# Performance work log

Hardware: AMD Instinct MI355X
Metric: run time of the kernel (lower is better)

The kernel has to match this reference:

```python
import jax, jax.numpy as jnp
import numpy as np

R = 8
EPS = 1e-08


def diff_x(t, r):
    # t: (B,C,H,W), running cumsum along H -> windowed sum along H
    left = t[:, :, r:2 * r + 1]
    middle = t[:, :, 2 * r + 1:] - t[:, :, :-2 * r - 1]
    right = t[:, :, -1:] - t[:, :, -2 * r - 1:-r - 1]
    return jnp.concatenate([left, middle, right], axis=2)


def diff_y(t, r):
    left = t[:, :, :, r:2 * r + 1]
    middle = t[:, :, :, 2 * r + 1:] - t[:, :, :, :-2 * r - 1]
    right = t[:, :, :, -1:] - t[:, :, :, -2 * r - 1:-r - 1]
    return jnp.concatenate([left, middle, right], axis=3)


def box_filter(x, r):
    return diff_y(diff_x(jnp.cumsum(x, axis=2), r).cumsum(axis=3), r)


def bilinear_align_corners(x, H, W):
    # x: (B,C,h,w) -> (B,C,H,W), matching F.interpolate(mode='bilinear', align_corners=True)
    h, w = x.shape[2], x.shape[3]
    ys = jnp.linspace(0.0, h - 1.0, H, dtype=x.dtype)
    xs = jnp.linspace(0.0, w - 1.0, W, dtype=x.dtype)
    y0 = jnp.clip(jnp.floor(ys).astype(jnp.int32), 0, h - 1)
    x0 = jnp.clip(jnp.floor(xs).astype(jnp.int32), 0, w - 1)
    y1 = jnp.clip(y0 + 1, 0, h - 1)
    x1 = jnp.clip(x0 + 1, 0, w - 1)
    wy = (ys - y0.astype(x.dtype))[:, None]   # (H,1)
    wx = (xs - x0.astype(x.dtype))[None, :]   # (1,W)
    v00 = x[:, :, y0[:, None], x0[None, :]]
    v01 = x[:, :, y0[:, None], x1[None, :]]
    v10 = x[:, :, y1[:, None], x0[None, :]]
    v11 = x[:, :, y1[:, None], x1[None, :]]
    top = v00 * (1 - wx) + v01 * wx
    bot = v10 * (1 - wx) + v11 * wx
    return top * (1 - wy) + bot * wy


def setup_inputs() -> dict:
    key = jax.random.key(0)
    k1, k2, k3 = jax.random.split(key, 3)
    lr_x = jax.random.uniform(k1, (4, 3, 512, 512), dtype=jnp.float32)
    lr_y = jax.random.uniform(k2, (4, 3, 512, 512), dtype=jnp.float32)
    hr_x = jax.random.uniform(k3, (4, 3, 2048, 2048), dtype=jnp.float32)
    return {"lr_x": lr_x, "lr_y": lr_y, "hr_x": hr_x}


def reference(lr_x, lr_y, hr_x):
    _, _, h_lr, w_lr = lr_x.shape
    _, _, h_hr, w_hr = hr_x.shape
    N = box_filter(jnp.ones((1, 1, h_lr, w_lr), dtype=lr_x.dtype), R)
    mean_x = box_filter(lr_x, R) / N
    mean_y = box_filter(lr_y, R) / N
    cov_xy = box_filter(lr_x * lr_y, R) / N - mean_x * mean_y
    var_x = box_filter(lr_x * lr_x, R) / N - mean_x * mean_x
    A = cov_xy / (var_x + EPS)
    b = mean_y - A * mean_x
    mean_A = bilinear_align_corners(A, h_hr, w_hr)
    mean_b = bilinear_align_corners(b, h_hr, w_hr)
    return mean_A * hr_x + mean_b
```

## Files before the change

### kernel.cpp

```cpp
#include <hip/hip_runtime.h>

#define RR 8
#define TILE 32
#define EXT (TILE + 2 * RR)

typedef float f4 __attribute__((ext_vector_type(4)));

__global__ __launch_bounds__(256) void k_ab(
    const float* __restrict__ lrx, const float* __restrict__ lry,
    float* __restrict__ Aout, float* __restrict__ Bout, int H, int W) {
  __shared__ float sx[EXT][EXT];
  __shared__ float sy[EXT][EXT];
  __shared__ float hx[EXT][TILE];
  __shared__ float hy[EXT][TILE];
  __shared__ float hxy[EXT][TILE];
  __shared__ float hxx[EXT][TILE];

  const int bc = blockIdx.z;
  const size_t plane = (size_t)bc * H * W;
  const float* __restrict__ px = lrx + plane;
  const float* __restrict__ py = lry + plane;
  const int tx0 = blockIdx.x * TILE;
  const int ty0 = blockIdx.y * TILE;
  const int tid = threadIdx.y * 32 + threadIdx.x;

  const bool interior = (tx0 >= RR) && (ty0 >= RR) &&
                        (tx0 + TILE + RR <= W) && (ty0 + TILE + RR <= H);
  if (interior) {
    const size_t base = (size_t)(ty0 - RR) * W + (tx0 - RR);
    for (int i = tid; i < EXT * (EXT / 4); i += 256) {
      int r = i / (EXT / 4);
      int c4 = (i - r * (EXT / 4)) * 4;
      size_t o = base + (size_t)r * W + c4;
      *(float4*)&sx[r][c4] = *(const float4*)(px + o);
      *(float4*)&sy[r][c4] = *(const float4*)(py + o);
    }
  } else {
    for (int i = tid; i < EXT * EXT; i += 256) {
      int r = i / EXT, c = i % EXT;
      int gy = ty0 + r - RR, gx = tx0 + c - RR;
      float vx = 0.f, vy = 0.f;
      if (gy >= 0 && gy < H && gx >= 0 && gx < W) {
        size_t o = (size_t)gy * W + gx;
        vx = px[o];
        vy = py[o];
      }
      sx[r][c] = vx;
      sy[r][c] = vy;
    }
  }
  __syncthreads();

  for (int q = tid; q < EXT * (TILE / 4); q += 256) {
    int r = q >> 3;
    int c0 = (q & 7) * 4;
    float xv[20], yv[20];
#pragma unroll
    for (int t = 0; t < 5; ++t) {
      float4 x4 = *(const float4*)&sx[r][c0 + 4 * t];
      float4 y4 = *(const float4*)&sy[r][c0 + 4 * t];
      xv[4 * t + 0] = x4.x; xv[4 * t + 1] = x4.y; xv[4 * t + 2] = x4.z; xv[4 * t + 3] = x4.w;
      yv[4 * t + 0] = y4.x; yv[4 * t + 1] = y4.y; yv[4 * t + 2] = y4.z; yv[4 * t + 3] = y4.w;
    }
    float pv[20], qv[20];
#pragma unroll
    for (int i = 0; i < 20; ++i) { pv[i] = xv[i] * yv[i]; qv[i] = xv[i] * xv[i]; }
    float ax = 0.f, ay = 0.f, axy = 0.f, axx = 0.f;
#pragma unroll
    for (int i = 0; i < 17; ++i) { ax += xv[i]; ay += yv[i]; axy += pv[i]; axx += qv[i]; }
    float4 ox, oy, oxy, oxx;
    ox.x = ax; oy.x = ay; oxy.x = axy; oxx.x = axx;
#pragma unroll
    for (int j = 1; j < 4; ++j) {
      ax += xv[j + 16] - xv[j - 1];
      ay += yv[j + 16] - yv[j - 1];
      axy += pv[j + 16] - pv[j - 1];
      axx += qv[j + 16] - qv[j - 1];
      (&ox.x)[j] = ax; (&oy.x)[j] = ay; (&oxy.x)[j] = axy; (&oxx.x)[j] = axx;
    }
    *(float4*)&hx[r][c0] = ox;
    *(float4*)&hy[r][c0] = oy;
    *(float4*)&hxy[r][c0] = oxy;
    *(float4*)&hxx[r][c0] = oxx;
  }
  __syncthreads();

  const int c = threadIdx.x;
  const int r0 = threadIdx.y * 4;
  float vx[20], vy[20], vxy[20], vxx[20];
#pragma unroll
  for (int i = 0; i < 20; ++i) {
    vx[i] = hx[r0 + i][c];
    vy[i] = hy[r0 + i][c];
    vxy[i] = hxy[r0 + i][c];
    vxx[i] = hxx[r0 + i][c];
  }
  float sX = 0.f, sY = 0.f, sXY = 0.f, sXX = 0.f;
#pragma unroll
  for (int i = 0; i < 17; ++i) { sX += vx[i]; sY += vy[i]; sXY += vxy[i]; sXX += vxx[i]; }

  const int gx = tx0 + c;
  const int nx = min(gx + RR, W - 1) - max(gx - RR, 0) + 1;
#pragma unroll
  for (int j = 0; j < 4; ++j) {
    if (j > 0) {
      sX += vx[j + 16] - vx[j - 1];
      sY += vy[j + 16] - vy[j - 1];
      sXY += vxy[j + 16] - vxy[j - 1];
      sXX += vxx[j + 16] - vxx[j - 1];
    }
    const int gy = ty0 + r0 + j;
    const int ny = min(gy + RR, H - 1) - max(gy - RR, 0) + 1;
    float inv = 1.f / (float)(nx * ny);
    float mx = sX * inv;
    float my = sY * inv;
    float cov = sXY * inv - mx * my;
    float var = sXX * inv - mx * mx;
    float a = cov / (var + 1e-8f);
    float bv = my - a * mx;
    size_t o = plane + (size_t)gy * W + gx;
    Aout[o] = a;
    Bout[o] = bv;
  }
}

#define KO_LDSW 264
__global__ __launch_bounds__(256) void k_out(
    const float* __restrict__ A, const float* __restrict__ Bb,
    const float* __restrict__ hr, float* __restrict__ out,
    int hl, int wl, int Hh, int Wh) {
  __shared__ float As[3][KO_LDSW];
  __shared__ float Bs[3][KO_LDSW];

  const int yb = blockIdx.y * 4;
  const int bc = blockIdx.z;
  const int xb = blockIdx.x * 1024;

  const float scy = (float)(hl - 1) / (float)(Hh - 1);
  const float scx = (float)(wl - 1) / (float)(Wh - 1);

  int v;
  {
    float fy0 = (float)yb * scy;
    int t = (int)fy0;
    if (t > hl - 1) t = hl - 1;
    v = t;
  }

  int ry0[4], ry1[4];
  float wyv[4];
#pragma unroll
  for (int r = 0; r < 4; ++r) {
    float fy = (float)(yb + r) * scy;
    int y0 = (int)fy;
    if (y0 > hl - 1) y0 = hl - 1;
    int y1 = y0 + 1;
    if (y1 > hl - 1) y1 = hl - 1;
    wyv[r] = fy - (float)y0;
    ry0[r] = y0 - v;
    ry1[r] = y1 - v;
  }

  const int x0base = (int)((float)xb * scx);
  const size_t lrBase = (size_t)bc * hl * wl;

  for (int i = threadIdx.x; i < 3 * KO_LDSW; i += 256) {
    int rr = i / KO_LDSW;
    int cc = i - rr * KO_LDSW;
    int xl = x0base + cc;
    if (xl > wl - 1) xl = wl - 1;
    int yr = v + rr;
    if (yr > hl - 1) yr = hl - 1;
    size_t o = lrBase + (size_t)yr * wl + xl;
    As[rr][cc] = A[o];
    Bs[rr][cc] = Bb[o];
  }
  __syncthreads();

  const int xg = xb + threadIdx.x * 4;
  int li[4];
  float wxv[4];
#pragma unroll
  for (int j = 0; j < 4; ++j) {
    float fx = (float)(xg + j) * scx;
    int x0 = (int)fx;
    wxv[j] = fx - (float)x0;
    li[j] = x0 - x0base;
  }

  const size_t hrBase = ((size_t)bc * Hh + yb) * Wh + xg;
  f4 h[4];
#pragma unroll
  for (int r = 0; r < 4; ++r)
    h[r] = __builtin_nontemporal_load((const f4*)(hr + hrBase + (size_t)r * Wh));

#pragma unroll
  for (int r = 0; r < 4; ++r) {
    const float* __restrict__ a0 = As[ry0[r]];
    const float* __restrict__ a1 = As[ry1[r]];
    const float* __restrict__ b0 = Bs[ry0[r]];
    const float* __restrict__ b1 = Bs[ry1[r]];
    const float wy = wyv[r];
    f4 res;
#pragma unroll
    for (int j = 0; j < 4; ++j) {
      int l = li[j];
      float w = wxv[j];
      float a00 = a0[l], a01 = a0[l + 1];
      float a10 = a1[l], a11 = a1[l + 1];
      float c00 = b0[l], c01 = b0[l + 1];
      float c10 = b1[l], c11 = b1[l + 1];
      float at = a00 + (a01 - a00) * w;
      float ab = a10 + (a11 - a10) * w;
      float bt = c00 + (c01 - c00) * w;
      float bbv = c10 + (c11 - c10) * w;
      float a = at + (ab - at) * wy;
      float b = bt + (bbv - bt) * wy;
      res[j] = a * h[r][j] + b;
    }
    __builtin_nontemporal_store(res, (f4*)(out + hrBase + (size_t)r * Wh));
  }
}

extern "C" void kernel_launch(void* const* d_in, const int* in_sizes, int n_in,
                              void* d_out, int out_size, void* d_ws, size_t ws_size,
                              hipStream_t stream) {
  const float* lrx = (const float*)d_in[0];
  const float* lry = (const float*)d_in[1];
  const float* hrx = (const float*)d_in[2];
  float* out = (float*)d_out;

  const int BC = 12;
  const int hl = 512, wl = 512;
  const int Hh = 2048, Wh = 2048;

  float* A = (float*)d_ws;
  float* B = A + (size_t)BC * hl * wl;

  dim3 g1(wl / TILE, hl / TILE, BC);
  dim3 b1(32, 8);
  k_ab<<<g1, b1, 0, stream>>>(lrx, lry, A, B, hl, wl);

  dim3 g2(Wh / 1024, Hh / 4, BC);
  dim3 b2(256);
  k_out<<<g2, b2, 0, stream>>>(A, B, hrx, out, hl, wl, Hh, Wh);
}
```

Before: 359.7 us.

## Interleave A/b coefficients, process 8 output rows per block, issue hr loads before barrier

```diff
diff --git a/kernel.cpp b/kernel.cpp
--- a/kernel.cpp
+++ b/kernel.cpp
@@ -8,7 +8,7 @@
 
 __global__ __launch_bounds__(256) void k_ab(
     const float* __restrict__ lrx, const float* __restrict__ lry,
-    float* __restrict__ Aout, float* __restrict__ Bout, int H, int W) {
+    float2* __restrict__ ABout, int H, int W) {
   __shared__ float sx[EXT][EXT];
   __shared__ float sy[EXT][EXT];
   __shared__ float hx[EXT][TILE];
@@ -119,63 +119,39 @@
     float a = cov / (var + 1e-8f);
     float bv = my - a * mx;
     size_t o = plane + (size_t)gy * W + gx;
-    Aout[o] = a;
-    Bout[o] = bv;
+    ABout[o] = make_float2(a, bv);
   }
 }
 
+#define ROWS 8
 #define KO_LDSW 264
 __global__ __launch_bounds__(256) void k_out(
-    const float* __restrict__ A, const float* __restrict__ Bb,
-    const float* __restrict__ hr, float* __restrict__ out,
-    int hl, int wl, int Hh, int Wh) {
-  __shared__ float As[3][KO_LDSW];
-  __shared__ float Bs[3][KO_LDSW];
-
-  const int yb = blockIdx.y * 4;
+    const float2* __restrict__ AB, const float* __restrict__ hr,
+    float* __restrict__ out, int hl, int wl, int Hh, int Wh) {
+  __shared__ float2 ABs[4][KO_LDSW];
+
+  const int yb = blockIdx.y * ROWS;
   const int bc = blockIdx.z;
   const int xb = blockIdx.x * 1024;
 
   const float scy = (float)(hl - 1) / (float)(Hh - 1);
   const float scx = (float)(wl - 1) / (float)(Wh - 1);
 
-  int v;
-  {
-    float fy0 = (float)yb * scy;
-    int t = (int)fy0;
-    if (t > hl - 1) t = hl - 1;
-    v = t;
-  }
-
-  int ry0[4], ry1[4];
-  float wyv[4];
-#pragma unroll
-  for (int r = 0; r < 4; ++r) {
-    float fy = (float)(yb + r) * scy;
-    int y0 = (int)fy;
-    if (y0 > hl - 1) y0 = hl - 1;
-    int y1 = y0 + 1;
-    if (y1 > hl - 1) y1 = hl - 1;
-    wyv[r] = fy - (float)y0;
-    ry0[r] = y0 - v;
-    ry1[r] = y1 - v;
-  }
+  int v = (int)((float)yb * scy);
+  if (v > hl - 1) v = hl - 1;
 
   const int x0base = (int)((float)xb * scx);
   const size_t lrBase = (size_t)bc * hl * wl;
 
-  for (int i = threadIdx.x; i < 3 * KO_LDSW; i += 256) {
+  for (int i = threadIdx.x; i < 4 * KO_LDSW; i += 256) {
     int rr = i / KO_LDSW;
     int cc = i - rr * KO_LDSW;
     int xl = x0base + cc;
     if (xl > wl - 1) xl = wl - 1;
     int yr = v + rr;
     if (yr > hl - 1) yr = hl - 1;
-    size_t o = lrBase + (size_t)yr * wl + xl;
-    As[rr][cc] = A[o];
-    Bs[rr][cc] = Bb[o];
-  }
-  __syncthreads();
+    ABs[rr][cc] = AB[lrBase + (size_t)yr * wl + xl];
+  }
 
   const int xg = xb + threadIdx.x * 4;
   int li[4];
@@ -189,36 +165,39 @@
   }
 
   const size_t hrBase = ((size_t)bc * Hh + yb) * Wh + xg;
-  f4 h[4];
-#pragma unroll
-  for (int r = 0; r < 4; ++r)
+  f4 h[ROWS];
+#pragma unroll
+  for (int r = 0; r < ROWS; ++r)
     h[r] = __builtin_nontemporal_load((const f4*)(hr + hrBase + (size_t)r * Wh));
 
-#pragma unroll
-  for (int r = 0; r < 4; ++r) {
-    const float* __restrict__ a0 = As[ry0[r]];
-    const float* __restrict__ a1 = As[ry1[r]];
-    const float* __restrict__ b0 = Bs[ry0[r]];
-    const float* __restrict__ b1 = Bs[ry1[r]];
-    const float wy = wyv[r];
+  __syncthreads();
+
+#pragma unroll
+  for (int r = 0; r < ROWS; ++r) {
+    float fy = (float)(yb + r) * scy;
+    int y0 = (int)fy;
+    if (y0 > hl - 1) y0 = hl - 1;
+    int y1 = y0 + 1;
+    if (y1 > hl - 1) y1 = hl - 1;
+    const float wy = fy - (float)y0;
+    const float2* __restrict__ R0 = ABs[y0 - v];
+    const float2* __restrict__ R1 = ABs[y1 - v];
     f4 res;
 #pragma unroll
     for (int j = 0; j < 4; ++j) {
       int l = li[j];
       float w = wxv[j];
-      float a00 = a0[l], a01 = a0[l + 1];
-      float a10 = a1[l], a11 = a1[l + 1];
-      float c00 = b0[l], c01 = b0[l + 1];
-      float c10 = b1[l], c11 = b1[l + 1];
-      float at = a00 + (a01 - a00) * w;
-      float ab = a10 + (a11 - a10) * w;
-      float bt = c00 + (c01 - c00) * w;
-      float bbv = c10 + (c11 - c10) * w;
+      float2 p00 = R0[l], p01 = R0[l + 1];
+      float2 p10 = R1[l], p11 = R1[l + 1];
+      float at = p00.x + (p01.x - p00.x) * w;
+      float ab = p10.x + (p11.x - p10.x) * w;
+      float bt = p00.y + (p01.y - p00.y) * w;
+      float bb = p10.y + (p11.y - p10.y) * w;
       float a = at + (ab - at) * wy;
-      float b = bt + (bbv - bt) * wy;
+      float b = bt + (bb - bt) * wy;
       res[j] = a * h[r][j] + b;
     }
-    __builtin_nontemporal_store(res, (f4*)(out + hrBase + (size_t)r * Wh));
+    *(f4*)(out + hrBase + (size_t)r * Wh) = res;
   }
 }
 
@@ -234,14 +213,13 @@
   const int hl = 512, wl = 512;
   const int Hh = 2048, Wh = 2048;
 
-  float* A = (float*)d_ws;
-  float* B = A + (size_t)BC * hl * wl;
+  float2* AB = (float2*)d_ws;
 
   dim3 g1(wl / TILE, hl / TILE, BC);
   dim3 b1(32, 8);
-  k_ab<<<g1, b1, 0, stream>>>(lrx, lry, A, B, hl, wl);
-
-  dim3 g2(Wh / 1024, Hh / 4, BC);
+  k_ab<<<g1, b1, 0, stream>>>(lrx, lry, AB, hl, wl);
+
+  dim3 g2(Wh / 1024, Hh / ROWS, BC);
   dim3 b2(256);
-  k_out<<<g2, b2, 0, stream>>>(A, B, hrx, out, hl, wl, Hh, Wh);
+  k_out<<<g2, b2, 0, stream>>>(AB, hrx, out, hl, wl, Hh, Wh);
 }
```

Measured after the change: 364.0 us. About the same (+1.2%).
